# Performance work log

Hardware: AMD Instinct MI355X
Metric: run time of the kernel (lower is better)

Reference implementation:

```python
import jax, jax.numpy as jnp
import numpy as np

B, N, E, ED, H, HID, OUT = 128, 100, 3200, 8, 4, 16, 32


def _ln(x, g, b):
    m = x.mean(-1, keepdims=True)
    v = ((x - m) ** 2).mean(-1, keepdims=True)
    return (x - m) / jnp.sqrt(v + 1e-5) * g + b


def _seg_softmax(logits, seg, n):
    # logits: [Etot, H], seg: [Etot] target node ids
    m = jax.ops.segment_max(logits, seg, num_segments=n)
    ex = jnp.exp(logits - m[seg])
    s = jax.ops.segment_sum(ex, seg, num_segments=n)
    return ex / (s[seg] + 1e-16)


def _tconv(x, src, dst, ea, Wq, bq, Wk, bk, Wv, bv, We, Ws, bs, heads, ch, n):
    # PyG TransformerConv, concat=False, root_weight=True, beta=False
    q = (x @ Wq.T + bq).reshape(-1, heads, ch)
    k = (x @ Wk.T + bk).reshape(-1, heads, ch)
    v = (x @ Wv.T + bv).reshape(-1, heads, ch)
    e = (ea @ We.T).reshape(-1, heads, ch)
    alpha = (q[dst] * (k[src] + e)).sum(-1) / jnp.sqrt(jnp.float32(ch))  # [Etot,H]
    alpha = _seg_softmax(alpha, dst, n)
    msg = (v[src] + e) * alpha[..., None]
    out = jax.ops.segment_sum(msg, dst, num_segments=n)  # [n,H,ch]
    out = out.mean(axis=1)  # concat=False -> head mean
    return out + x @ Ws.T + bs


def setup_inputs() -> dict:
    key = jax.random.key(0)
    ks = jax.random.split(key, 32)
    d = {}
    d['nodes_feats'] = jax.random.randint(ks[0], (B, N, 1), 0, 5).astype(jnp.float32)
    d['edge_index'] = jax.random.randint(ks[1], (B, 2, E), 0, N).astype(jnp.int32)
    d['edge_attr'] = jax.random.normal(ks[2], (B, E, ED), jnp.float32)
    d['agent_id'] = jax.random.randint(ks[3], (B, 1), 0, N).astype(jnp.int32)
    s = 0.1
    d['entity_embed'] = jax.random.normal(ks[4], (5, 4), jnp.float32)
    d['W1'] = jax.random.normal(ks[5], (HID, 4 + ED), jnp.float32) * s
    d['b1'] = jnp.zeros((HID,), jnp.float32)
    d['W2'] = jax.random.normal(ks[6], (HID, HID), jnp.float32) * s
    d['b2'] = jnp.zeros((HID,), jnp.float32)
    d['W3'] = jax.random.normal(ks[7], (HID, HID), jnp.float32) * s
    d['b3'] = jnp.zeros((HID,), jnp.float32)
    d['ln_g'] = jnp.ones((HID,), jnp.float32)
    d['ln_b'] = jnp.zeros((HID,), jnp.float32)
    i = 8
    for pre, ch, outd in (('g1', HID, HID), ('g2', OUT, OUT)):
        d[pre + '_Wq'] = jax.random.normal(ks[i + 0], (H * ch, HID), jnp.float32) * s
        d[pre + '_bq'] = jnp.zeros((H * ch,), jnp.float32)
        d[pre + '_Wk'] = jax.random.normal(ks[i + 1], (H * ch, HID), jnp.float32) * s
        d[pre + '_bk'] = jnp.zeros((H * ch,), jnp.float32)
        d[pre + '_Wv'] = jax.random.normal(ks[i + 2], (H * ch, HID), jnp.float32) * s
        d[pre + '_bv'] = jnp.zeros((H * ch,), jnp.float32)
        d[pre + '_We'] = jax.random.normal(ks[i + 3], (H * ch, ED), jnp.float32) * s
        d[pre + '_Ws'] = jax.random.normal(ks[i + 4], (outd, HID), jnp.float32) * s
        d[pre + '_bs'] = jnp.zeros((outd,), jnp.float32)
        i += 5
    return d


def reference(nodes_feats, edge_index, edge_attr, agent_id, entity_embed,
              W1, b1, W2, b2, W3, b3, ln_g, ln_b,
              g1_Wq, g1_bq, g1_Wk, g1_bk, g1_Wv, g1_bv, g1_We, g1_Ws, g1_bs,
              g2_Wq, g2_bq, g2_Wk, g2_bk, g2_Wv, g2_bv, g2_We, g2_Ws, g2_bs):
    n_tot = B * N
    # batched graph -> flat graph with per-batch node offsets
    offs = (jnp.arange(B, dtype=edge_index.dtype) * N)[:, None, None]
    ei = (edge_index + offs).transpose(1, 0, 2).reshape(2, -1)  # [2, B*E]
    src, dst = ei[0], ei[1]
    x = nodes_feats.reshape(-1, 1)            # [n_tot, 1]
    ea = edge_attr.reshape(-1, ED)            # [B*E, ED]

    # Embedding message-passing layer (aggr='add')
    etype = x[:, 0].astype(jnp.int32)[src]
    emb = entity_embed[etype]                  # [Etot, 4]
    h = jnp.concatenate([emb, ea], axis=1)
    h = _ln(jax.nn.relu(h @ W1.T + b1), ln_g, ln_b)
    h = _ln(jax.nn.relu(h @ W2.T + b2), ln_g, ln_b)
    h = _ln(jax.nn.relu(h @ W3.T + b3), ln_g, ln_b)
    z = jax.ops.segment_sum(h, dst, num_segments=n_tot)  # [n_tot, 16]

    a = _tconv(z, src, dst, ea, g1_Wq, g1_bq, g1_Wk, g1_bk, g1_Wv, g1_bv,
               g1_We, g1_Ws, g1_bs, H, HID, n_tot)
    a = _tconv(a, src, dst, ea, g2_Wq, g2_bq, g2_Wk, g2_bk, g2_Wv, g2_bv,
               g2_We, g2_Ws, g2_bs, H, OUT, n_tot)
    a = jax.nn.relu(a).reshape(B, N, OUT)
    # graph_aggr == 'agent': gather the agent node per batch
    out = jnp.take_along_axis(a, agent_id[:, :, None].astype(jnp.int32), axis=1)
    return out[:, 0, :]  # [B, OUT]
```

## Files before the change

### kernel.cpp

```cpp
#include <hip/hip_runtime.h>
#include <math.h>
#include <stdint.h>

#define Bb   128
#define Nn   100
#define Ee   3200
#define NTOT (Bb*Nn)
#define ETOT (Bb*Ee)



__global__ __launch_bounds__(512) void k_csr(const int* __restrict__ ei,
                                             const int* __restrict__ agent,
                                             int* __restrict__ off,
                                             int2* __restrict__ cpair,
                                             int* __restrict__ mark)
{
    int b = ((blockIdx.x & 7) << 4) + (blockIdx.x >> 3);
    int t = threadIdx.x;
    __shared__ int s_src[Ee];
    __shared__ int s_dst[Ee];
    __shared__ int cnt[128];
    __shared__ int exc[128];
    __shared__ int cur[128];
    if (t < 128) cnt[t] = 0;
    if (t < Nn) mark[b * Nn + t] = 0;
    __syncthreads();
    const int* eis = ei + (size_t)b * 2 * Ee;
    const int* eid = eis + Ee;
    for (int e = t; e < Ee; e += 512) {
        int s = eis[e];
        int d = eid[e];
        s_src[e] = s;
        s_dst[e] = d;
        atomicAdd(&cnt[d], 1);
    }
    __syncthreads();
    if (t < 128) exc[t] = cnt[t];
    __syncthreads();
    for (int d = 1; d < 128; d <<= 1) {
        int v = 0;
        if (t < 128 && t >= d) v = exc[t - d];
        __syncthreads();
        if (t < 128) exc[t] += v;
        __syncthreads();
    }
    if (t < 128) { int e0 = exc[t] - cnt[t]; exc[t] = e0; cur[t] = e0; }
    __syncthreads();
    if (t < Nn) off[b * Nn + t] = b * Ee + exc[t];
    if (b == Bb - 1 && t == 0) off[NTOT] = ETOT;
    for (int e = t; e < Ee; e += 512) {
        int d = s_dst[e];
        int idx = atomicAdd(&cur[d], 1);
        cpair[b * Ee + idx] = make_int2(s_src[e] + b * Nn, b * Ee + e);
    }
    int an = agent[b];
    if (t == 0) mark[b * Nn + an] = 1;
    for (int e = t; e < Ee; e += 512) {
        if (s_dst[e] == an) mark[b * Nn + s_src[e]] = 1;
    }
}


__device__ __forceinline__ void ln_reg(float* h, const float* __restrict__ g,
                                       const float* __restrict__ b) {
    float s = 0.f;
#pragma unroll
    for (int c = 0; c < 16; c++) s += h[c];
    float m = s * 0.0625f;
    float v = 0.f;
#pragma unroll
    for (int c = 0; c < 16; c++) { float d = h[c] - m; v += d * d; }
    float r = rsqrtf(v * 0.0625f + 1e-5f);
#pragma unroll
    for (int c = 0; c < 16; c++) h[c] = (h[c] - m) * r * g[c] + b[c];
}

__global__ __launch_bounds__(256) void k_mlpz(
    const float* __restrict__ nf, const float* __restrict__ ea, const float* __restrict__ ee,
    const float* __restrict__ W1, const float* __restrict__ b1,
    const float* __restrict__ W2, const float* __restrict__ b2,
    const float* __restrict__ W3, const float* __restrict__ b3,
    const float* __restrict__ lg, const float* __restrict__ lb,
    const float* __restrict__ Wk, const float* __restrict__ bk,
    const float* __restrict__ Wv, const float* __restrict__ bv,
    const int* __restrict__ off, const int2* __restrict__ cpair,
    float* __restrict__ z, float* __restrict__ k1, float* __restrict__ v1)
{
    __shared__ float hs[4][64][17];
    __shared__ int sdeg[4];
    int lane = threadIdx.x & 63;
    int wid  = threadIdx.x >> 6;
    int n    = (blockIdx.x & 7) * (NTOT / 8) + (blockIdx.x >> 3) * 4 + wid;

    int o0 = off[n];
    int deg = off[n + 1] - o0;
    if (lane == 0) sdeg[wid] = deg;
    __syncthreads();
    int mdeg = max(max(sdeg[0], sdeg[1]), max(sdeg[2], sdeg[3]));
    int chunks = (mdeg + 63) >> 6;

    float zp = 0.f;
    for (int ch = 0; ch < chunks; ch++) {
        int i = ch * 64 + lane;
        float h3[16];
        if (i < deg) {
            int2 p = cpair[o0 + i];
            int et = (int)nf[p.x];
            float in[12];
#pragma unroll
            for (int j = 0; j < 4; j++) in[j] = ee[et * 4 + j];
            const float4* ea4 = (const float4*)(ea + (size_t)p.y * 8);
            float4 ua = ea4[0], ub = ea4[1];
            in[4] = ua.x; in[5] = ua.y; in[6] = ua.z; in[7] = ua.w;
            in[8] = ub.x; in[9] = ub.y; in[10] = ub.z; in[11] = ub.w;

            float h1[16];
#pragma unroll
            for (int c = 0; c < 16; c++) {
                float s = b1[c];
#pragma unroll
                for (int j = 0; j < 12; j++) s = fmaf(W1[c * 12 + j], in[j], s);
                h1[c] = fmaxf(s, 0.f);
            }
            ln_reg(h1, lg, lb);
            float h2[16];
#pragma unroll
            for (int c = 0; c < 16; c++) {
                float s = b2[c];
#pragma unroll
                for (int j = 0; j < 16; j++) s = fmaf(W2[c * 16 + j], h1[j], s);
                h2[c] = fmaxf(s, 0.f);
            }
            ln_reg(h2, lg, lb);
#pragma unroll
            for (int c = 0; c < 16; c++) {
                float s = b3[c];
#pragma unroll
                for (int j = 0; j < 16; j++) s = fmaf(W3[c * 16 + j], h2[j], s);
                h3[c] = fmaxf(s, 0.f);
            }
            ln_reg(h3, lg, lb);
        } else {
#pragma unroll
            for (int c = 0; c < 16; c++) h3[c] = 0.f;
        }
#pragma unroll
        for (int c = 0; c < 16; c++) hs[wid][lane][c] = h3[c];
        __syncthreads();
        int g = lane >> 4, c = lane & 15;
        float s = 0.f;
#pragma unroll
        for (int k = 0; k < 16; k++) s += hs[wid][g * 16 + k][c];
        s += __shfl_xor(s, 16);
        s += __shfl_xor(s, 32);
        zp += s;
        __syncthreads();
    }

    if (lane < 16) z[n * 16 + lane] = zp;

    float ak = bk[lane], av = bv[lane];
#pragma unroll
    for (int j = 0; j < 16; j++) {
        float zj = __shfl(zp, j, 16);
        ak = fmaf(Wk[lane * 16 + j], zj, ak);
        av = fmaf(Wv[lane * 16 + j], zj, av);
    }
    k1[n * 64 + lane] = ak;
    v1[n * 64 + lane] = av;
}


__global__ __launch_bounds__(256) void k_attn1(
    const float* __restrict__ ea,
    const float* __restrict__ k1, const float* __restrict__ v1,
    const float* __restrict__ z, const int* __restrict__ mark,
    const float* __restrict__ Wq, const float* __restrict__ bq,
    const float* __restrict__ We, const float* __restrict__ Ws, const float* __restrict__ bs,
    const int* __restrict__ off, const int2* __restrict__ cpair,
    float* __restrict__ a1)
{
    int n = (blockIdx.x & 7) * (NTOT / 8) + (blockIdx.x >> 3);
    if (!mark[n]) return;

    __shared__ float sm[4][64], sl[4][64], sa[4][64];
    int lane = threadIdx.x & 63;
    int w    = threadIdx.x >> 6;

    float zz[16];
#pragma unroll
    for (int j = 0; j < 16; j++) zz[j] = z[n * 16 + j];
    float ql = bq[lane];
#pragma unroll
    for (int j = 0; j < 16; j++) ql = fmaf(Wq[lane * 16 + j], zz[j], ql);
    float wer[8];
#pragma unroll
    for (int j = 0; j < 8; j++) wer[j] = We[lane * 8 + j];

    int o0  = off[n];
    int deg = off[n + 1] - o0;
    int i    = o0 + ((deg * w) >> 2);
    int iend = o0 + ((deg * (w + 1)) >> 2);

    float m = -1e30f, l = 0.f, acc = 0.f;
    for (; i + 2 <= iend; i += 2) {
        int2 pA = cpair[i];
        int2 pB = cpair[i + 1];
        const float4* eaA = (const float4*)(ea + (size_t)pA.y * 8);
        const float4* eaB = (const float4*)(ea + (size_t)pB.y * 8);
        float4 a0v = eaA[0], a1v = eaA[1], b0v = eaB[0], b1v = eaB[1];
        float eA = wer[0] * a0v.x + wer[1] * a0v.y + wer[2] * a0v.z + wer[3] * a0v.w
                 + wer[4] * a1v.x + wer[5] * a1v.y + wer[6] * a1v.z + wer[7] * a1v.w;
        float eB = wer[0] * b0v.x + wer[1] * b0v.y + wer[2] * b0v.z + wer[3] * b0v.w
                 + wer[4] * b1v.x + wer[5] * b1v.y + wer[6] * b1v.z + wer[7] * b1v.w;
        float kA = k1[(size_t)pA.x * 64 + lane];
        float kB = k1[(size_t)pB.x * 64 + lane];
        float vA = v1[(size_t)pA.x * 64 + lane];
        float vB = v1[(size_t)pB.x * 64 + lane];
        float tA = ql * (kA + eA);
        float tB = ql * (kB + eB);
        tA += __shfl_xor(tA, 1, 16);  tB += __shfl_xor(tB, 1, 16);
        tA += __shfl_xor(tA, 2, 16);  tB += __shfl_xor(tB, 2, 16);
        tA += __shfl_xor(tA, 4, 16);  tB += __shfl_xor(tB, 4, 16);
        tA += __shfl_xor(tA, 8, 16);  tB += __shfl_xor(tB, 8, 16);
        float lA  = tA * 0.25f;
        float lBv = tB * 0.25f;
        float nm = fmaxf(m, fmaxf(lA, lBv));
        float sc = __expf(m - nm);
        float wA = __expf(lA - nm);
        float wB = __expf(lBv - nm);
        acc = acc * sc + wA * (vA + eA) + wB * (vB + eB);
        l   = l * sc + wA + wB;
        m   = nm;
    }
    for (; i < iend; i++) {
        int2 p = cpair[i];
        const float4* ea4 = (const float4*)(ea + (size_t)p.y * 8);
        float4 u0 = ea4[0], u1 = ea4[1];
        float el = wer[0] * u0.x + wer[1] * u0.y + wer[2] * u0.z + wer[3] * u0.w
                 + wer[4] * u1.x + wer[5] * u1.y + wer[6] * u1.z + wer[7] * u1.w;
        float kl = k1[(size_t)p.x * 64 + lane];
        float tq = ql * (kl + el);
        tq += __shfl_xor(tq, 1, 16);
        tq += __shfl_xor(tq, 2, 16);
        tq += __shfl_xor(tq, 4, 16);
        tq += __shfl_xor(tq, 8, 16);
        float logit = tq * 0.25f;
        float nm = fmaxf(m, logit);
        float sc = __expf(m - nm);
        float wv = __expf(logit - nm);
        float vl = v1[(size_t)p.x * 64 + lane];
        acc = acc * sc + wv * (vl + el);
        l   = l * sc + wv;
        m   = nm;
    }
    sm[w][lane] = m; sl[w][lane] = l; sa[w][lane] = acc;
    __syncthreads();
    if (w == 0) {
        float M = fmaxf(fmaxf(sm[0][lane], sm[1][lane]), fmaxf(sm[2][lane], sm[3][lane]));
        float L = 0.f, A = 0.f;
#pragma unroll
        for (int ww = 0; ww < 4; ww++) {
            float sc = __expf(sm[ww][lane] - M);
            L += sc * sl[ww][lane];
            A += sc * sa[ww][lane];
        }
        float y = (deg > 0) ? (A / L) : 0.f;
        y += __shfl_xor(y, 16);
        y += __shfl_xor(y, 32);
        y *= 0.25f;
        if (lane < 16) {
            float r = bs[lane];
#pragma unroll
            for (int j = 0; j < 16; j++) r = fmaf(Ws[lane * 16 + j], zz[j], r);
            a1[n * 16 + lane] = y + r;
        }
    }
}


__global__ __launch_bounds__(512) void k_g2(
    const float* __restrict__ ea, const float* __restrict__ a1, const int* __restrict__ agent,
    const float* __restrict__ Wq, const float* __restrict__ bq,
    const float* __restrict__ Wk, const float* __restrict__ bk,
    const float* __restrict__ Wv, const float* __restrict__ bv,
    const float* __restrict__ We, const float* __restrict__ Ws, const float* __restrict__ bs,
    const int* __restrict__ off, const int2* __restrict__ cpair,
    float* __restrict__ out)
{
    __shared__ float sm[8][64], sl[8][64], sa0[8][64], sa1[8][64];
    int b = ((blockIdx.x & 7) << 4) + (blockIdx.x >> 3);
    int lane = threadIdx.x & 63;
    int w = threadIdx.x >> 6;
    int n = b * Nn + agent[b];
    int v0 = lane * 2, v1i = lane * 2 + 1;

    float aa[16];
#pragma unroll
    for (int j = 0; j < 16; j++) aa[j] = a1[n * 16 + j];

    float wk0[16], wk1[16], wv0[16], wv1[16], we0[8], we1[8];
#pragma unroll
    for (int j = 0; j < 16; j++) {
        wk0[j] = Wk[v0 * 16 + j];  wk1[j] = Wk[v1i * 16 + j];
        wv0[j] = Wv[v0 * 16 + j];  wv1[j] = Wv[v1i * 16 + j];
    }
#pragma unroll
    for (int j = 0; j < 8; j++) { we0[j] = We[v0 * 8 + j]; we1[j] = We[v1i * 8 + j]; }

    float q0 = bq[v0], q1v = bq[v1i];
#pragma unroll
    for (int j = 0; j < 16; j++) {
        q0  = fmaf(Wq[v0 * 16 + j],  aa[j], q0);
        q1v = fmaf(Wq[v1i * 16 + j], aa[j], q1v);
    }

    int o0 = off[n];
    int deg = off[n + 1] - o0;

    float m = -1e30f, l = 0.f, a0 = 0.f, a1c = 0.f;
    for (int i = w; i < deg; i += 8) {
        int2 p = cpair[o0 + i];
        int src = p.x, ge = p.y;
        float as[16];
#pragma unroll
        for (int j = 0; j < 16; j++) as[j] = a1[src * 16 + j];
        const float4* ea4 = (const float4*)(ea + (size_t)ge * 8);
        float4 u0 = ea4[0], u1 = ea4[1];
        float eav[8] = {u0.x, u0.y, u0.z, u0.w, u1.x, u1.y, u1.z, u1.w};

        float k0 = bk[v0], k1v = bk[v1i], vv0 = bv[v0], vv1 = bv[v1i];
#pragma unroll
        for (int j = 0; j < 16; j++) {
            k0  = fmaf(wk0[j], as[j], k0);
            k1v = fmaf(wk1[j], as[j], k1v);
            vv0 = fmaf(wv0[j], as[j], vv0);
            vv1 = fmaf(wv1[j], as[j], vv1);
        }
        float e0 = 0.f, e1 = 0.f;
#pragma unroll
        for (int j = 0; j < 8; j++) { e0 = fmaf(we0[j], eav[j], e0); e1 = fmaf(we1[j], eav[j], e1); }

        float t = q0 * (k0 + e0) + q1v * (k1v + e1);
        t += __shfl_xor(t, 1, 16);
        t += __shfl_xor(t, 2, 16);
        t += __shfl_xor(t, 4, 16);
        t += __shfl_xor(t, 8, 16);
        float logit = t * 0.17677669529663687f;
        float nm = fmaxf(m, logit);
        float sc = __expf(m - nm);
        float wgt = __expf(logit - nm);
        a0  = a0 * sc + wgt * (vv0 + e0);
        a1c = a1c * sc + wgt * (vv1 + e1);
        l   = l * sc + wgt;
        m   = nm;
    }
    sm[w][lane] = m; sl[w][lane] = l; sa0[w][lane] = a0; sa1[w][lane] = a1c;
    __syncthreads();
    if (w == 0) {
        float M = sm[0][lane];
#pragma unroll
        for (int ww = 1; ww < 8; ww++) M = fmaxf(M, sm[ww][lane]);
        float L = 0.f, A0 = 0.f, A1 = 0.f;
#pragma unroll
        for (int ww = 0; ww < 8; ww++) {
            float sc = __expf(sm[ww][lane] - M);
            L  += sc * sl[ww][lane];
            A0 += sc * sa0[ww][lane];
            A1 += sc * sa1[ww][lane];
        }
        float y0 = (deg > 0) ? (A0 / L) : 0.f;
        float y1 = (deg > 0) ? (A1 / L) : 0.f;
        y0 += __shfl_xor(y0, 16); y0 += __shfl_xor(y0, 32);
        y1 += __shfl_xor(y1, 16); y1 += __shfl_xor(y1, 32);
        y0 *= 0.25f; y1 *= 0.25f;

        if (lane < 16) {
            int c0 = lane * 2, c1 = lane * 2 + 1;
            float r0 = bs[c0], r1 = bs[c1];
#pragma unroll
            for (int j = 0; j < 16; j++) {
                r0 = fmaf(Ws[c0 * 16 + j], aa[j], r0);
                r1 = fmaf(Ws[c1 * 16 + j], aa[j], r1);
            }
            out[b * 32 + c0] = fmaxf(y0 + r0, 0.f);
            out[b * 32 + c1] = fmaxf(y1 + r1, 0.f);
        }
    }
}


extern "C" void kernel_launch(void* const* d_in, const int* in_sizes, int n_in,
                              void* d_out, int out_size, void* d_ws, size_t ws_size,
                              hipStream_t stream) {
    (void)in_sizes; (void)n_in; (void)out_size; (void)ws_size;
    const float* nf    = (const float*)d_in[0];
    const int*   ei    = (const int*)d_in[1];
    const float* ea    = (const float*)d_in[2];
    const int*   agent = (const int*)d_in[3];
    const float* ee    = (const float*)d_in[4];
    const float* W1    = (const float*)d_in[5];
    const float* b1    = (const float*)d_in[6];
    const float* W2    = (const float*)d_in[7];
    const float* b2    = (const float*)d_in[8];
    const float* W3    = (const float*)d_in[9];
    const float* b3    = (const float*)d_in[10];
    const float* lg    = (const float*)d_in[11];
    const float* lb    = (const float*)d_in[12];
    const float* g1Wq  = (const float*)d_in[13];
    const float* g1bq  = (const float*)d_in[14];
    const float* g1Wk  = (const float*)d_in[15];
    const float* g1bk  = (const float*)d_in[16];
    const float* g1Wv  = (const float*)d_in[17];
    const float* g1bv  = (const float*)d_in[18];
    const float* g1We  = (const float*)d_in[19];
    const float* g1Ws  = (const float*)d_in[20];
    const float* g1bs  = (const float*)d_in[21];
    const float* g2Wq  = (const float*)d_in[22];
    const float* g2bq  = (const float*)d_in[23];
    const float* g2Wk  = (const float*)d_in[24];
    const float* g2bk  = (const float*)d_in[25];
    const float* g2Wv  = (const float*)d_in[26];
    const float* g2bv  = (const float*)d_in[27];
    const float* g2We  = (const float*)d_in[28];
    const float* g2Ws  = (const float*)d_in[29];
    const float* g2bs  = (const float*)d_in[30];
    float* out = (float*)d_out;

    char* w = (char*)d_ws;
    int* mark  = (int*)w;  w += (size_t)NTOT * 4;
    int* off   = (int*)w;  w += (size_t)(NTOT + 4) * 4;
    w = (char*)(((uintptr_t)w + 15) & ~(uintptr_t)15);
    int2* cpair = (int2*)w; w += (size_t)ETOT * 8;
    float* z   = (float*)w; w += (size_t)NTOT * 16 * 4;
    float* k1  = (float*)w; w += (size_t)NTOT * 64 * 4;
    float* v1  = (float*)w; w += (size_t)NTOT * 64 * 4;
    float* a1  = (float*)w; w += (size_t)NTOT * 16 * 4;

    k_csr<<<dim3(Bb), dim3(512), 0, stream>>>(ei, agent, off, cpair, mark);
    k_mlpz<<<dim3(NTOT / 4), dim3(256), 0, stream>>>(
        nf, ea, ee, W1, b1, W2, b2, W3, b3, lg, lb,
        g1Wk, g1bk, g1Wv, g1bv,
        off, cpair, z, k1, v1);
    k_attn1<<<dim3(NTOT), dim3(256), 0, stream>>>(
        ea, k1, v1, z, mark,
        g1Wq, g1bq, g1We, g1Ws, g1bs,
        off, cpair, a1);
    k_g2<<<dim3(Bb), dim3(512), 0, stream>>>(
        ea, a1, agent, g2Wq, g2bq, g2Wk, g2bk, g2Wv, g2bv, g2We, g2Ws, g2bs,
        off, cpair, out);
}
```

Baseline: 194.8 us.

## Use wave shuffles for CSR scan and per-node edge reduction; widen CSR blocks

The CSR build kernel now runs 1024 threads per graph and replaces the barrier-heavy shared-memory prefix scan with a single-wave shuffle scan, two counts per lane. The MLP/segment-sum kernel drops the shared-memory staging and block-wide barriers. Each wave now loops only over its own node's degree and reduces the 16 channels with butterfly shuffles, so every lane holds the full z vector for the K/V projection. This removes sync stalls and load imbalance across the waves in a block, at the cost of 96 shuffles per chunk instead of shared-memory adds.

```diff
diff --git a/kernel.cpp b/kernel.cpp
--- a/kernel.cpp
+++ b/kernel.cpp
@@ -10,11 +10,11 @@
 
 
 
-__global__ __launch_bounds__(512) void k_csr(const int* __restrict__ ei,
-                                             const int* __restrict__ agent,
-                                             int* __restrict__ off,
-                                             int2* __restrict__ cpair,
-                                             int* __restrict__ mark)
+__global__ __launch_bounds__(1024) void k_csr(const int* __restrict__ ei,
+                                              const int* __restrict__ agent,
+                                              int* __restrict__ off,
+                                              int2* __restrict__ cpair,
+                                              int* __restrict__ mark)
 {
     int b = ((blockIdx.x & 7) << 4) + (blockIdx.x >> 3);
     int t = threadIdx.x;
@@ -28,7 +28,7 @@
     __syncthreads();
     const int* eis = ei + (size_t)b * 2 * Ee;
     const int* eid = eis + Ee;
-    for (int e = t; e < Ee; e += 512) {
+    for (int e = t; e < Ee; e += 1024) {
         int s = eis[e];
         int d = eid[e];
         s_src[e] = s;
@@ -36,27 +36,31 @@
         atomicAdd(&cnt[d], 1);
     }
     __syncthreads();
-    if (t < 128) exc[t] = cnt[t];
-    __syncthreads();
-    for (int d = 1; d < 128; d <<= 1) {
-        int v = 0;
-        if (t < 128 && t >= d) v = exc[t - d];
-        __syncthreads();
-        if (t < 128) exc[t] += v;
-        __syncthreads();
-    }
-    if (t < 128) { int e0 = exc[t] - cnt[t]; exc[t] = e0; cur[t] = e0; }
+    if (t < 64) {
+        int c0 = cnt[2 * t];
+        int c1 = cnt[2 * t + 1];
+        int p = c0 + c1;
+#pragma unroll
+        for (int d = 1; d < 64; d <<= 1) {
+            int v = __shfl_up(p, d);
+            if (t >= d) p += v;
+        }
+        exc[2 * t]     = p - c0 - c1;
+        exc[2 * t + 1] = p - c1;
+        cur[2 * t]     = p - c0 - c1;
+        cur[2 * t + 1] = p - c1;
+    }
     __syncthreads();
     if (t < Nn) off[b * Nn + t] = b * Ee + exc[t];
     if (b == Bb - 1 && t == 0) off[NTOT] = ETOT;
-    for (int e = t; e < Ee; e += 512) {
+    for (int e = t; e < Ee; e += 1024) {
         int d = s_dst[e];
         int idx = atomicAdd(&cur[d], 1);
         cpair[b * Ee + idx] = make_int2(s_src[e] + b * Nn, b * Ee + e);
     }
     int an = agent[b];
     if (t == 0) mark[b * Nn + an] = 1;
-    for (int e = t; e < Ee; e += 512) {
+    for (int e = t; e < Ee; e += 1024) {
         if (s_dst[e] == an) mark[b * Nn + s_src[e]] = 1;
     }
 }
@@ -87,20 +91,18 @@
     const int* __restrict__ off, const int2* __restrict__ cpair,
     float* __restrict__ z, float* __restrict__ k1, float* __restrict__ v1)
 {
-    __shared__ float hs[4][64][17];
-    __shared__ int sdeg[4];
     int lane = threadIdx.x & 63;
     int wid  = threadIdx.x >> 6;
     int n    = (blockIdx.x & 7) * (NTOT / 8) + (blockIdx.x >> 3) * 4 + wid;
 
     int o0 = off[n];
     int deg = off[n + 1] - o0;
-    if (lane == 0) sdeg[wid] = deg;
-    __syncthreads();
-    int mdeg = max(max(sdeg[0], sdeg[1]), max(sdeg[2], sdeg[3]));
-    int chunks = (mdeg + 63) >> 6;
-
-    float zp = 0.f;
+    int chunks = (deg + 63) >> 6;
+
+    float zs[16];
+#pragma unroll
+    for (int c = 0; c < 16; c++) zs[c] = 0.f;
+
     for (int ch = 0; ch < chunks; ch++) {
         int i = ch * 64 + lane;
         float h3[16];
@@ -146,26 +148,26 @@
             for (int c = 0; c < 16; c++) h3[c] = 0.f;
         }
 #pragma unroll
-        for (int c = 0; c < 16; c++) hs[wid][lane][c] = h3[c];
-        __syncthreads();
-        int g = lane >> 4, c = lane & 15;
-        float s = 0.f;
-#pragma unroll
-        for (int k = 0; k < 16; k++) s += hs[wid][g * 16 + k][c];
-        s += __shfl_xor(s, 16);
-        s += __shfl_xor(s, 32);
-        zp += s;
-        __syncthreads();
-    }
-
-    if (lane < 16) z[n * 16 + lane] = zp;
+        for (int c = 0; c < 16; c++) {
+            float s = h3[c];
+            s += __shfl_xor(s, 1);
+            s += __shfl_xor(s, 2);
+            s += __shfl_xor(s, 4);
+            s += __shfl_xor(s, 8);
+            s += __shfl_xor(s, 16);
+            s += __shfl_xor(s, 32);
+            zs[c] += s;
+        }
+    }
+
+#pragma unroll
+    for (int c = 0; c < 16; c++) if (lane == c) z[n * 16 + c] = zs[c];
 
     float ak = bk[lane], av = bv[lane];
 #pragma unroll
     for (int j = 0; j < 16; j++) {
-        float zj = __shfl(zp, j, 16);
-        ak = fmaf(Wk[lane * 16 + j], zj, ak);
-        av = fmaf(Wv[lane * 16 + j], zj, av);
+        ak = fmaf(Wk[lane * 16 + j], zs[j], ak);
+        av = fmaf(Wv[lane * 16 + j], zs[j], av);
     }
     k1[n * 64 + lane] = ak;
     v1[n * 64 + lane] = av;
@@ -438,7 +440,7 @@
     float* v1  = (float*)w; w += (size_t)NTOT * 64 * 4;
     float* a1  = (float*)w; w += (size_t)NTOT * 16 * 4;
 
-    k_csr<<<dim3(Bb), dim3(512), 0, stream>>>(ei, agent, off, cpair, mark);
+    k_csr<<<dim3(Bb), dim3(1024), 0, stream>>>(ei, agent, off, cpair, mark);
     k_mlpz<<<dim3(NTOT / 4), dim3(256), 0, stream>>>(
         nf, ea, ee, W1, b1, W2, b2, W3, b3, lg, lb,
         g1Wk, g1bk, g1Wv, g1bv,
```

New measurement: 193.7 us. Within noise of the previous version (-0.6%).
